# Kernel optimization log

Measured on AMD Instinct MI355X. Metric: run time of the kernel, lower is better.

The kernel has to match this reference:

```python
import jax, jax.numpy as jnp
import numpy as np

BETA = 0.1
IGNORE_INDEX = -100
B, T, H, V = 4, 512, 2048, 32000


def setup_inputs() -> dict:
    key = jax.random.key(0)
    k1, k2, k3, k4, k5 = jax.random.split(key, 5)
    x = jax.random.normal(k1, (B, T, H), dtype=jnp.float32)
    ref_x = jax.random.normal(k2, (B, T, H), dtype=jnp.float32)
    y = jax.random.randint(k3, (B, T), 0, V, dtype=jnp.int64)
    W = jax.random.normal(k4, (V, H), dtype=jnp.float32) * 0.02
    ref_W = jax.random.normal(k5, (V, H), dtype=jnp.float32) * 0.02
    return {"x": x, "ref_x": ref_x, "y": y, "W": W, "ref_W": ref_W}


def _avg_logps(inp, weight, target):
    # inp: [B,T,H], weight: [V,H], target: [B,T]
    logits = jnp.einsum('bth,vh->btv', inp, weight)          # [B,T,V]
    lse = jax.nn.logsumexp(logits, axis=-1)                  # [B,T]
    mask = (target != IGNORE_INDEX)
    safe = jnp.where(mask, target, 0)
    tok = jnp.take_along_axis(logits, safe[..., None], axis=-1)[..., 0]
    per_token_logps = tok - lse                               # [B,T]
    mask_f = mask.astype(per_token_logps.dtype)
    return (per_token_logps * mask_f).sum(-1) / mask_f.sum(-1)  # [B]


def reference(x, ref_x, y, W, ref_W):
    half = y.shape[0] // 2
    policy_logps = _avg_logps(x, W, y)
    # reference model runs under no_grad in the original
    ref_logps = jax.lax.stop_gradient(_avg_logps(ref_x, ref_W, y))
    logratios = policy_logps - ref_logps                      # [B]
    kl = jnp.zeros((), dtype=logratios.dtype)                 # kl=None -> 0
    chosen_losses = 1.0 - jax.nn.sigmoid(BETA * (logratios[:half] - kl))
    rejected_losses = 1.0 - jax.nn.sigmoid(BETA * (kl - logratios[half:]))
    return (chosen_losses.sum() + rejected_losses.sum()) / half
```

## Files before the change

kernel.cpp:

```cpp
#include <hip/hip_runtime.h>
#include <stdint.h>

#define B_DIM 4
#define T_DIM 512
#define NTOK  2048
#define H_DIM 2048
#define V_DIM 32000
#define TM    128
#define TN    128
#define BK    64
#define NCHUNK (V_DIM / TN)
#define NTILE  (NTOK / TM)
#define BETA   0.1f
#define IGNORE_INDEX (-100)

typedef _Float16 f16;
typedef _Float16 half8 __attribute__((ext_vector_type(8)));
typedef float    f32x4 __attribute__((ext_vector_type(4)));

__global__ __launch_bounds__(256) void cvt_f32_f16(const float* __restrict__ src,
                                                   f16* __restrict__ dst, int n) {
    int i = (blockIdx.x * 256 + threadIdx.x) * 8;
    if (i + 8 > n) return;
    float4 v0 = *(const float4*)(src + i);
    float4 v1 = *(const float4*)(src + i + 4);
    half8 h = { (f16)v0.x, (f16)v0.y, (f16)v0.z, (f16)v0.w,
                (f16)v1.x, (f16)v1.y, (f16)v1.z, (f16)v1.w };
    *(half8*)(dst + i) = h;
}

template <bool DIRECT>
__global__ __launch_bounds__(256, 3) void gemm_lse(
    const void* __restrict__ x0, const void* __restrict__ x1,
    const void* __restrict__ w0, const void* __restrict__ w1,
    const int* __restrict__ y,
    float2* __restrict__ pMS,
    float* __restrict__ tokL)
{
    const int tile  = blockIdx.x;
    const int chunk = blockIdx.y;
    const int model = blockIdx.z;
    const void* Xp = model ? x1 : x0;
    const void* Wp = model ? w1 : w0;

    const int tid  = threadIdx.x;
    const int lane = tid & 63;
    const int wave = tid >> 6;
    const int wm   = wave >> 1;
    const int wn   = wave & 1;

    __shared__ __align__(16) f16 As[8][TM][8];
    __shared__ __align__(16) f16 Bs[8][TN][8];
    __shared__ float redM[TM][2];
    __shared__ float redS[TM][2];
    __shared__ int   ys[TM];

    if (tid < TM) ys[tid] = y[tile * TM + tid];

    f32x4 acc[4][4];
#pragma unroll
    for (int i = 0; i < 4; ++i)
#pragma unroll
        for (int j = 0; j < 4; ++j) acc[i][j] = (f32x4){0.f, 0.f, 0.f, 0.f};

    const int rowA0 = tile * TM;
    const int rowB0 = chunk * TN;
    const int kc    = lane >> 4;

    const int rS = tid & 127;
    const int cS = tid >> 7;

    if (DIRECT) {
        const f16* pA = (const f16*)Xp + (size_t)(rowA0 + rS) * H_DIM + cS * 8;
        const f16* pB = (const f16*)Wp + (size_t)(rowB0 + rS) * H_DIM + cS * 8;
        f16* dA = &As[0][0][0] + tid * 8;
        f16* dB = &Bs[0][0][0] + tid * 8;

        for (int k0 = 0; k0 < H_DIM; k0 += BK) {
#pragma unroll
            for (int i = 0; i < 4; ++i)
                __builtin_amdgcn_global_load_lds(
                    (const __attribute__((address_space(1))) unsigned int*)(pA + i * 16),
                    (__attribute__((address_space(3))) unsigned int*)(dA + i * 2048),
                    16, 0, 0);
#pragma unroll
            for (int i = 0; i < 4; ++i)
                __builtin_amdgcn_global_load_lds(
                    (const __attribute__((address_space(1))) unsigned int*)(pB + i * 16),
                    (__attribute__((address_space(3))) unsigned int*)(dB + i * 2048),
                    16, 0, 0);
            pA += BK; pB += BK;
            __syncthreads();

#pragma unroll
            for (int p = 0; p < 2; ++p) {
                half8 af[4], bfr[4];
#pragma unroll
                for (int i = 0; i < 4; ++i)
                    af[i] = *(const half8*)As[p * 4 + kc][wm * 64 + i * 16 + (lane & 15)];
#pragma unroll
                for (int j = 0; j < 4; ++j)
                    bfr[j] = *(const half8*)Bs[p * 4 + kc][wn * 64 + j * 16 + (lane & 15)];
#pragma unroll
                for (int i = 0; i < 4; ++i)
#pragma unroll
                    for (int j = 0; j < 4; ++j)
                        acc[i][j] = __builtin_amdgcn_mfma_f32_16x16x32_f16(af[i], bfr[j], acc[i][j], 0, 0, 0);
            }
            __syncthreads();
        }
    } else {
        const float* pA = (const float*)Xp + (size_t)(rowA0 + rS) * H_DIM + cS * 8;
        const float* pB = (const float*)Wp + (size_t)(rowB0 + rS) * H_DIM + cS * 8;
        f16* dA = &As[0][0][0] + tid * 8;
        f16* dB = &Bs[0][0][0] + tid * 8;

        for (int k0 = 0; k0 < H_DIM; k0 += BK) {
#pragma unroll
            for (int i = 0; i < 4; ++i) {
                float4 v0 = *(const float4*)(pA + i * 16);
                float4 v1 = *(const float4*)(pA + i * 16 + 4);
                half8 h = { (f16)v0.x, (f16)v0.y, (f16)v0.z, (f16)v0.w,
                            (f16)v1.x, (f16)v1.y, (f16)v1.z, (f16)v1.w };
                *(half8*)(dA + i * 2048) = h;
            }
#pragma unroll
            for (int i = 0; i < 4; ++i) {
                float4 v0 = *(const float4*)(pB + i * 16);
                float4 v1 = *(const float4*)(pB + i * 16 + 4);
                half8 h = { (f16)v0.x, (f16)v0.y, (f16)v0.z, (f16)v0.w,
                            (f16)v1.x, (f16)v1.y, (f16)v1.z, (f16)v1.w };
                *(half8*)(dB + i * 2048) = h;
            }
            pA += BK; pB += BK;
            __syncthreads();

#pragma unroll
            for (int p = 0; p < 2; ++p) {
                half8 af[4], bfr[4];
#pragma unroll
                for (int i = 0; i < 4; ++i)
                    af[i] = *(const half8*)As[p * 4 + kc][wm * 64 + i * 16 + (lane & 15)];
#pragma unroll
                for (int j = 0; j < 4; ++j)
                    bfr[j] = *(const half8*)Bs[p * 4 + kc][wn * 64 + j * 16 + (lane & 15)];
#pragma unroll
                for (int i = 0; i < 4; ++i)
#pragma unroll
                    for (int j = 0; j < 4; ++j)
                        acc[i][j] = __builtin_amdgcn_mfma_f32_16x16x32_f16(af[i], bfr[j], acc[i][j], 0, 0, 0);
            }
            __syncthreads();
        }
    }

#pragma unroll
    for (int i = 0; i < 4; ++i) {
#pragma unroll
        for (int r = 0; r < 4; ++r) {
            int rl = wm * 64 + i * 16 + ((lane >> 4) << 2) + r;
            int t = ys[rl];
            int trel = t - (rowB0 + wn * 64);
#pragma unroll
            for (int j = 0; j < 4; ++j) {
                if (trel == j * 16 + (lane & 15))
                    tokL[model * NTOK + rowA0 + rl] = acc[i][j][r];
            }
        }
    }

#pragma unroll
    for (int i = 0; i < 4; ++i) {
#pragma unroll
        for (int r = 0; r < 4; ++r) {
            float mx = fmaxf(fmaxf(acc[i][0][r], acc[i][1][r]),
                             fmaxf(acc[i][2][r], acc[i][3][r]));
            for (int m = 1; m < 16; m <<= 1) mx = fmaxf(mx, __shfl_xor(mx, m, 64));
            float s = 0.f;
#pragma unroll
            for (int j = 0; j < 4; ++j) s += __expf(acc[i][j][r] - mx);
            for (int m = 1; m < 16; m <<= 1) s += __shfl_xor(s, m, 64);
            if ((lane & 15) == 0) {
                int rl = wm * 64 + i * 16 + ((lane >> 4) << 2) + r;
                redM[rl][wn] = mx;
                redS[rl][wn] = s;
            }
        }
    }
    __syncthreads();
    if (tid < TM) {
        float m0 = redM[tid][0], m1 = redM[tid][1];
        float s0 = redS[tid][0], s1 = redS[tid][1];
        float M = fmaxf(m0, m1);
        float S = s0 * __expf(m0 - M) + s1 * __expf(m1 - M);
        size_t o = ((size_t)model * NTOK + rowA0 + tid) * NCHUNK + chunk;
        pMS[o] = make_float2(M, S);
    }
}

__global__ __launch_bounds__(256) void lse_reduce(const float2* __restrict__ pMS,
                                                  const float* __restrict__ tokL,
                                                  const int* __restrict__ y,
                                                  float* __restrict__ logp) {
    int g = blockIdx.x * 4 + (threadIdx.x >> 6);
    int lane = threadIdx.x & 63;
    const float2* base = pMS + (size_t)g * NCHUNK;
    float M = -1e30f, S = 0.f;
    for (int c = lane; c < NCHUNK; c += 64) {
        float2 ms = base[c];
        if (ms.x > M) { S = S * __expf(M - ms.x) + ms.y; M = ms.x; }
        else          { S += ms.y * __expf(ms.x - M); }
    }
#pragma unroll
    for (int off = 1; off < 64; off <<= 1) {
        float Mo = __shfl_xor(M, off, 64);
        float So = __shfl_xor(S, off, 64);
        float Mn = fmaxf(M, Mo);
        S = S * __expf(M - Mn) + So * __expf(Mo - Mn);
        M = Mn;
    }
    if (lane == 0) {
        float lse = M + logf(S);
        int token = g & (NTOK - 1);
        int t = y[token];
        logp[g] = (t == IGNORE_INDEX) ? 0.f : (tokL[g] - lse);
    }
}

__device__ __forceinline__ float sigf(float z) { return 1.f / (1.f + expf(-z)); }

__global__ void final_loss(const float* __restrict__ logp,
                           const int* __restrict__ y,
                           float* __restrict__ out) {
    int lane = threadIdx.x;
    float avg[2][4];
    for (int model = 0; model < 2; ++model)
        for (int b = 0; b < 4; ++b) {
            float s = 0.f, c = 0.f;
            for (int t = lane; t < T_DIM; t += 64) {
                int token = b * T_DIM + t;
                if (y[token] != IGNORE_INDEX) { s += logp[model * NTOK + token]; c += 1.f; }
            }
            for (int m = 1; m < 64; m <<= 1) {
                s += __shfl_xor(s, m, 64);
                c += __shfl_xor(c, m, 64);
            }
            avg[model][b] = s / c;
        }
    if (lane == 0) {
        float loss = 0.f;
        for (int b = 0; b < 2; ++b) {
            float lr = avg[0][b] - avg[1][b];
            loss += 1.f - sigf(BETA * lr);
        }
        for (int b = 2; b < 4; ++b) {
            float lr = avg[0][b] - avg[1][b];
            loss += 1.f - sigf(-BETA * lr);
        }
        out[0] = loss * 0.5f;
    }
}

extern "C" void kernel_launch(void* const* d_in, const int* in_sizes, int n_in,
                              void* d_out, int out_size, void* d_ws, size_t ws_size,
                              hipStream_t stream) {
    const float* x  = (const float*)d_in[0];
    const float* rx = (const float*)d_in[1];
    const int*   y  = (const int*)d_in[2];
    const float* W  = (const float*)d_in[3];
    const float* rW = (const float*)d_in[4];
    float* out = (float*)d_out;

    const size_t nX = (size_t)NTOK * H_DIM;
    const size_t nW = (size_t)V_DIM * H_DIM;

    char* p = (char*)d_ws;
    float2* pMS = (float2*)p; p += (size_t)2 * NTOK * NCHUNK * 8;
    float* tokL = (float*)p;  p += (size_t)2 * NTOK * 4;
    float* logp = (float*)p;  p += (size_t)2 * NTOK * 4;
    size_t base = (size_t)(p - (char*)d_ws);
    size_t need_fast = base + 2 * nX * 2 + 2 * nW * 2;

    dim3 grid(NTILE, NCHUNK, 2);
    if (ws_size >= need_fast) {
        f16* xb  = (f16*)p; p += nX * 2;
        f16* rxb = (f16*)p; p += nX * 2;
        f16* wb  = (f16*)p; p += nW * 2;
        f16* rwb = (f16*)p; p += nW * 2;
        cvt_f32_f16<<<(int)(nX / 8 / 256), 256, 0, stream>>>(x,  xb,  (int)nX);
        cvt_f32_f16<<<(int)(nX / 8 / 256), 256, 0, stream>>>(rx, rxb, (int)nX);
        cvt_f32_f16<<<(int)(nW / 8 / 256), 256, 0, stream>>>(W,  wb,  (int)nW);
        cvt_f32_f16<<<(int)(nW / 8 / 256), 256, 0, stream>>>(rW, rwb, (int)nW);
        gemm_lse<true><<<grid, 256, 0, stream>>>(xb, rxb, wb, rwb, y, pMS, tokL);
    } else {
        gemm_lse<false><<<grid, 256, 0, stream>>>(x, rx, W, rW, y, pMS, tokL);
    }
    lse_reduce<<<1024, 256, 0, stream>>>(pMS, tokL, y, logp);
    final_loss<<<1, 64, 0, stream>>>(logp, y, out);
}
```

Measured before the change: 1.566 ms.

## Rewrite fp16 GEMM-LSE as 256x256 tile, 8-wave double-buffered pipelined kernel

Replaces the 128x128, 4-wave fp16 GEMM with a 256x256 tile kernel using 512 threads. It double-buffers LDS and issues async global-to-LDS loads interleaved with MFMA phases, using explicit barriers, waitcnts and setprio. The block index is remapped so that blocks sharing a weight chunk are grouped, and per-chunk max/sum partials halve in count. This targets memory stalls and load/compute serialization, at the cost of large LDS use (128KB), heavy register pressure from 32 accumulators, and fragile hand scheduling.

```diff
diff --git a/kernel.cpp b/kernel.cpp
--- a/kernel.cpp
+++ b/kernel.cpp
@@ -6,17 +6,22 @@
 #define NTOK  2048
 #define H_DIM 2048
 #define V_DIM 32000
+#define BETA   0.1f
+#define IGNORE_INDEX (-100)
+
 #define TM    128
 #define TN    128
 #define BK    64
-#define NCHUNK (V_DIM / TN)
-#define NTILE  (NTOK / TM)
-#define BETA   0.1f
-#define IGNORE_INDEX (-100)
+#define NCHUNK 250
+#define NCH8  125
+#define NTILE8 8
 
 typedef _Float16 f16;
 typedef _Float16 half8 __attribute__((ext_vector_type(8)));
 typedef float    f32x4 __attribute__((ext_vector_type(4)));
+
+#define AS1(p) ((const __attribute__((address_space(1))) unsigned int*)(p))
+#define AS3(p) ((__attribute__((address_space(3))) unsigned int*)(p))
 
 __global__ __launch_bounds__(256) void cvt_f32_f16(const float* __restrict__ src,
                                                    f16* __restrict__ dst, int n) {
@@ -29,10 +34,183 @@
     *(half8*)(dst + i) = h;
 }
 
-template <bool DIRECT>
-__global__ __launch_bounds__(256, 3) void gemm_lse(
-    const void* __restrict__ x0, const void* __restrict__ x1,
-    const void* __restrict__ w0, const void* __restrict__ w1,
+
+#define DSR_(d, a, OFFSTR) \
+    asm volatile("ds_read_b128 %0, %1 offset:" OFFSTR : "=v"(d) : "v"(a))
+
+#define VM4    asm volatile("s_waitcnt vmcnt(4)" ::: "memory")
+#define VMNONE ((void)0)
+
+#define STAGE(MAT, BUF, KH, KT, PTR) do {                                      \
+    const f16* s_ = (PTR) + (((KT) & 31) << 6) + (KH) * 32;                    \
+    f16* d_ = dBase + (BUF) * 32768 + (MAT) * 16384 + (KH) * 8192;             \
+    __builtin_amdgcn_global_load_lds(AS1(s_),      AS3(d_),        16, 0, 0);  \
+    __builtin_amdgcn_global_load_lds(AS1(s_ + 16), AS3(d_ + 4096), 16, 0, 0);  \
+} while (0)
+
+#define PHASE(BUF, KH, FH, WAITV, ...) do {                                    \
+    half8 af[4];                                                               \
+    unsigned aAd = A_rd + ((BUF) * 65536u + (KH) * 16384u + (FH) * 1024u);     \
+    DSR_(af[0], aAd, "0");   DSR_(af[1], aAd, "256");                          \
+    DSR_(af[2], aAd, "512"); DSR_(af[3], aAd, "768");                          \
+    if ((FH) == 0) {                                                           \
+        unsigned bAd = B_rd + ((BUF) * 65536u + (KH) * 16384u);                \
+        DSR_(bfp[0], bAd, "0");   DSR_(bfp[1], bAd, "256");                    \
+        DSR_(bfp[2], bAd, "512"); DSR_(bfp[3], bAd, "768");                    \
+    }                                                                          \
+    __VA_ARGS__;                                                               \
+    __builtin_amdgcn_sched_barrier(0);                                         \
+    __builtin_amdgcn_s_barrier();                                              \
+    __builtin_amdgcn_sched_barrier(0);                                         \
+    asm volatile("s_waitcnt lgkmcnt(0)" ::: "memory");                         \
+    __builtin_amdgcn_sched_barrier(0);                                         \
+    __builtin_amdgcn_s_setprio(1);                                             \
+    _Pragma("unroll")                                                          \
+    for (int m_ = 0; m_ < 4; ++m_) {                                           \
+        _Pragma("unroll")                                                      \
+        for (int n_ = 0; n_ < 4; ++n_)                                         \
+            acc[(FH) * 4 + m_][n_] = __builtin_amdgcn_mfma_f32_16x16x32_f16(   \
+                af[m_], bfp[n_], acc[(FH) * 4 + m_][n_], 0, 0, 0);             \
+    }                                                                          \
+    __builtin_amdgcn_s_setprio(0);                                             \
+    __builtin_amdgcn_sched_barrier(0);                                         \
+    WAITV;                                                                     \
+    __builtin_amdgcn_s_barrier();                                              \
+    __builtin_amdgcn_sched_barrier(0);                                         \
+} while (0)
+
+__global__ __launch_bounds__(512, 2) void gemm_lse8(
+    const f16* __restrict__ x0, const f16* __restrict__ x1,
+    const f16* __restrict__ w0, const f16* __restrict__ w1,
+    const int* __restrict__ y,
+    float2* __restrict__ pMS,
+    float* __restrict__ tokL)
+{
+    const int orig = blockIdx.x;
+    const int wg   = (orig & 7) * 250 + (orig >> 3);
+    const int tile = wg & 7;
+    const int rest = wg >> 3;
+    const int chunk = rest % NCH8;
+    const int model = rest / NCH8;
+
+    const f16* Xp = model ? x1 : x0;
+    const f16* Wp = model ? w1 : w0;
+
+    const int tid  = threadIdx.x;
+    const int lane = tid & 63;
+    const int wave = tid >> 6;
+    const int wm   = wave >> 2;
+    const int wn   = wave & 3;
+
+    __shared__ __align__(16) f16 sm[2][2][8][256][8];
+    __shared__ float redM[256][4];
+    __shared__ float redS[256][4];
+    __shared__ int   ys[256];
+
+    const int rowA0 = tile * 256;
+    const int rowB0 = chunk * 256;
+
+    f32x4 acc[8][4];
+#pragma unroll
+    for (int i = 0; i < 8; ++i)
+#pragma unroll
+        for (int j = 0; j < 4; ++j) acc[i][j] = (f32x4){0.f, 0.f, 0.f, 0.f};
+
+    const int rS = tid & 255;
+    const int cS = tid >> 8;
+    const f16* pA = Xp + (size_t)(rowA0 + rS) * H_DIM + cS * 8;
+    const f16* pB = Wp + (size_t)(rowB0 + rS) * H_DIM + cS * 8;
+    f16* dBase = &sm[0][0][0][0][0] + (size_t)tid * 8;
+
+    auto* smp3 = (__attribute__((address_space(3))) f16*)&sm[0][0][0][0][0];
+    const unsigned smBase = (unsigned)(uintptr_t)smp3;
+    const unsigned A_rd = smBase + ((unsigned)(lane >> 4) << 12)
+                        + (((unsigned)(wm * 128 + (lane & 15))) << 4);
+    const unsigned B_rd = smBase + 32768u + ((unsigned)(lane >> 4) << 12)
+                        + (((unsigned)(wn * 64 + (lane & 15))) << 4);
+
+    half8 bfp[4];
+
+    int yreg = 0;
+    if (tid < 256) yreg = y[rowA0 + tid];
+    asm volatile("s_waitcnt vmcnt(0)" ::: "memory");
+    __builtin_amdgcn_sched_barrier(0);
+
+    STAGE(0, 0, 0, 0, pA); STAGE(1, 0, 0, 0, pB);
+    STAGE(0, 0, 1, 0, pA); STAGE(1, 0, 1, 0, pB);
+    STAGE(0, 1, 0, 1, pA); STAGE(1, 1, 0, 1, pB);
+    asm volatile("s_waitcnt vmcnt(4)" ::: "memory");
+    __builtin_amdgcn_sched_barrier(0);
+    __builtin_amdgcn_s_barrier();
+    __builtin_amdgcn_sched_barrier(0);
+    if (tid < 256) ys[tid] = yreg;
+
+#pragma unroll 1
+    for (int i = 0; i < 16; ++i) {
+        const int kt1 = 2 * i + 1, kt2 = 2 * i + 2, kt3 = 2 * i + 3;
+        PHASE(0, 0, 0, VMNONE, STAGE(0, 1, 1, kt1, pA));
+        PHASE(0, 0, 1, VMNONE, STAGE(1, 1, 1, kt1, pB));
+        PHASE(0, 1, 0, VMNONE, STAGE(0, 0, 0, kt2, pA));
+        PHASE(0, 1, 1, VM4,    STAGE(1, 0, 0, kt2, pB));
+        PHASE(1, 0, 0, VMNONE, STAGE(0, 0, 1, kt2, pA));
+        PHASE(1, 0, 1, VMNONE, STAGE(1, 0, 1, kt2, pB));
+        PHASE(1, 1, 0, VMNONE, STAGE(0, 1, 0, kt3, pA));
+        PHASE(1, 1, 1, VM4,    STAGE(1, 1, 0, kt3, pB));
+    }
+
+    __syncthreads();
+
+#pragma unroll
+    for (int i2 = 0; i2 < 8; ++i2) {
+#pragma unroll
+        for (int r = 0; r < 4; ++r) {
+            int rl = wm * 128 + i2 * 16 + ((lane >> 4) << 2) + r;
+            int t = ys[rl];
+            int trel = t - (rowB0 + wn * 64);
+#pragma unroll
+            for (int j = 0; j < 4; ++j) {
+                if (trel == j * 16 + (lane & 15))
+                    tokL[model * NTOK + rowA0 + rl] = acc[i2][j][r];
+            }
+        }
+    }
+
+#pragma unroll
+    for (int i2 = 0; i2 < 8; ++i2) {
+#pragma unroll
+        for (int r = 0; r < 4; ++r) {
+            float mx = fmaxf(fmaxf(acc[i2][0][r], acc[i2][1][r]),
+                             fmaxf(acc[i2][2][r], acc[i2][3][r]));
+            for (int m = 1; m < 16; m <<= 1) mx = fmaxf(mx, __shfl_xor(mx, m, 64));
+            float s = 0.f;
+#pragma unroll
+            for (int j = 0; j < 4; ++j) s += __expf(acc[i2][j][r] - mx);
+            for (int m = 1; m < 16; m <<= 1) s += __shfl_xor(s, m, 64);
+            if ((lane & 15) == 0) {
+                int rl = wm * 128 + i2 * 16 + ((lane >> 4) << 2) + r;
+                redM[rl][wn] = mx;
+                redS[rl][wn] = s;
+            }
+        }
+    }
+    __syncthreads();
+    if (tid < 256) {
+        float M = redM[tid][0], S = redS[tid][0];
+#pragma unroll
+        for (int q = 1; q < 4; ++q) {
+            float m2 = redM[tid][q], s2 = redS[tid][q];
+            float Mn = fmaxf(M, m2);
+            S = S * __expf(M - Mn) + s2 * __expf(m2 - Mn);
+            M = Mn;
+        }
+        size_t o = ((size_t)model * NTOK + rowA0 + tid) * NCH8 + chunk;
+        pMS[o] = make_float2(M, S);
+    }
+}
+
+__global__ __launch_bounds__(256, 3) void gemm_lse_f32(
+    const float* __restrict__ x0, const float* __restrict__ x1,
+    const float* __restrict__ w0, const float* __restrict__ w1,
     const int* __restrict__ y,
     float2* __restrict__ pMS,
     float* __restrict__ tokL)
@@ -40,8 +218,8 @@
     const int tile  = blockIdx.x;
     const int chunk = blockIdx.y;
     const int model = blockIdx.z;
-    const void* Xp = model ? x1 : x0;
-    const void* Wp = model ? w1 : w0;
+    const float* Xp = model ? x1 : x0;
+    const float* Wp = model ? w1 : w0;
 
     const int tid  = threadIdx.x;
     const int lane = tid & 63;
@@ -66,92 +244,50 @@
     const int rowA0 = tile * TM;
     const int rowB0 = chunk * TN;
     const int kc    = lane >> 4;
-
     const int rS = tid & 127;
     const int cS = tid >> 7;
 
-    if (DIRECT) {
-        const f16* pA = (const f16*)Xp + (size_t)(rowA0 + rS) * H_DIM + cS * 8;
-        const f16* pB = (const f16*)Wp + (size_t)(rowB0 + rS) * H_DIM + cS * 8;
-        f16* dA = &As[0][0][0] + tid * 8;
-        f16* dB = &Bs[0][0][0] + tid * 8;
-
-        for (int k0 = 0; k0 < H_DIM; k0 += BK) {
+    const float* pA = Xp + (size_t)(rowA0 + rS) * H_DIM + cS * 8;
+    const float* pB = Wp + (size_t)(rowB0 + rS) * H_DIM + cS * 8;
+    f16* dA = &As[0][0][0] + tid * 8;
+    f16* dB = &Bs[0][0][0] + tid * 8;
+
+    for (int k0 = 0; k0 < H_DIM; k0 += BK) {
+#pragma unroll
+        for (int i = 0; i < 4; ++i) {
+            float4 v0 = *(const float4*)(pA + i * 16);
+            float4 v1 = *(const float4*)(pA + i * 16 + 4);
+            half8 h = { (f16)v0.x, (f16)v0.y, (f16)v0.z, (f16)v0.w,
+                        (f16)v1.x, (f16)v1.y, (f16)v1.z, (f16)v1.w };
+            *(half8*)(dA + i * 2048) = h;
+        }
+#pragma unroll
+        for (int i = 0; i < 4; ++i) {
+            float4 v0 = *(const float4*)(pB + i * 16);
+            float4 v1 = *(const float4*)(pB + i * 16 + 4);
+            half8 h = { (f16)v0.x, (f16)v0.y, (f16)v0.z, (f16)v0.w,
+                        (f16)v1.x, (f16)v1.y, (f16)v1.z, (f16)v1.w };
+            *(half8*)(dB + i * 2048) = h;
+        }
+        pA += BK; pB += BK;
+        __syncthreads();
+
+#pragma unroll
+        for (int p = 0; p < 2; ++p) {
+            half8 af[4], bfr[4];
 #pragma unroll
             for (int i = 0; i < 4; ++i)
-                __builtin_amdgcn_global_load_lds(
-                    (const __attribute__((address_space(1))) unsigned int*)(pA + i * 16),
-                    (__attribute__((address_space(3))) unsigned int*)(dA + i * 2048),
-                    16, 0, 0);
+                af[i] = *(const half8*)As[p * 4 + kc][wm * 64 + i * 16 + (lane & 15)];
+#pragma unroll
+            for (int j = 0; j < 4; ++j)
+                bfr[j] = *(const half8*)Bs[p * 4 + kc][wn * 64 + j * 16 + (lane & 15)];
 #pragma unroll
             for (int i = 0; i < 4; ++i)
-                __builtin_amdgcn_global_load_lds(
-                    (const __attribute__((address_space(1))) unsigned int*)(pB + i * 16),
-                    (__attribute__((address_space(3))) unsigned int*)(dB + i * 2048),
-                    16, 0, 0);
-            pA += BK; pB += BK;
-            __syncthreads();
-
-#pragma unroll
-            for (int p = 0; p < 2; ++p) {
-                half8 af[4], bfr[4];
-#pragma unroll
-                for (int i = 0; i < 4; ++i)
-                    af[i] = *(const half8*)As[p * 4 + kc][wm * 64 + i * 16 + (lane & 15)];
 #pragma unroll
                 for (int j = 0; j < 4; ++j)
-                    bfr[j] = *(const half8*)Bs[p * 4 + kc][wn * 64 + j * 16 + (lane & 15)];
-#pragma unroll
-                for (int i = 0; i < 4; ++i)
-#pragma unroll
-                    for (int j = 0; j < 4; ++j)
-                        acc[i][j] = __builtin_amdgcn_mfma_f32_16x16x32_f16(af[i], bfr[j], acc[i][j], 0, 0, 0);
-            }
-            __syncthreads();
-        }
-    } else {
-        const float* pA = (const float*)Xp + (size_t)(rowA0 + rS) * H_DIM + cS * 8;
-        const float* pB = (const float*)Wp + (size_t)(rowB0 + rS) * H_DIM + cS * 8;
-        f16* dA = &As[0][0][0] + tid * 8;
-        f16* dB = &Bs[0][0][0] + tid * 8;
-
-        for (int k0 = 0; k0 < H_DIM; k0 += BK) {
-#pragma unroll
-            for (int i = 0; i < 4; ++i) {
-                float4 v0 = *(const float4*)(pA + i * 16);
-                float4 v1 = *(const float4*)(pA + i * 16 + 4);
-                half8 h = { (f16)v0.x, (f16)v0.y, (f16)v0.z, (f16)v0.w,
-                            (f16)v1.x, (f16)v1.y, (f16)v1.z, (f16)v1.w };
-                *(half8*)(dA + i * 2048) = h;
-            }
-#pragma unroll
-            for (int i = 0; i < 4; ++i) {
-                float4 v0 = *(const float4*)(pB + i * 16);
-                float4 v1 = *(const float4*)(pB + i * 16 + 4);
-                half8 h = { (f16)v0.x, (f16)v0.y, (f16)v0.z, (f16)v0.w,
-                            (f16)v1.x, (f16)v1.y, (f16)v1.z, (f16)v1.w };
-                *(half8*)(dB + i * 2048) = h;
-            }
-            pA += BK; pB += BK;
-            __syncthreads();
-
-#pragma unroll
-            for (int p = 0; p < 2; ++p) {
-                half8 af[4], bfr[4];
-#pragma unroll
-                for (int i = 0; i < 4; ++i)
-                    af[i] = *(const half8*)As[p * 4 + kc][wm * 64 + i * 16 + (lane & 15)];
-#pragma unroll
-                for (int j = 0; j < 4; ++j)
-                    bfr[j] = *(const half8*)Bs[p * 4 + kc][wn * 64 + j * 16 + (lane & 15)];
-#pragma unroll
-                for (int i = 0; i < 4; ++i)
-#pragma unroll
-                    for (int j = 0; j < 4; ++j)
-                        acc[i][j] = __builtin_amdgcn_mfma_f32_16x16x32_f16(af[i], bfr[j], acc[i][j], 0, 0, 0);
-            }
-            __syncthreads();
-        }
+                    acc[i][j] = __builtin_amdgcn_mfma_f32_16x16x32_f16(af[i], bfr[j], acc[i][j], 0, 0, 0);
+        }
+        __syncthreads();
     }
 
 #pragma unroll
@@ -193,7 +329,7 @@
         float s0 = redS[tid][0], s1 = redS[tid][1];
         float M = fmaxf(m0, m1);
         float S = s0 * __expf(m0 - M) + s1 * __expf(m1 - M);
-        size_t o = ((size_t)model * NTOK + rowA0 + tid) * NCHUNK + chunk;
+        size_t o = ((size_t)model * NTOK + tile * TM + tid) * NCHUNK + chunk;
         pMS[o] = make_float2(M, S);
     }
 }
@@ -201,12 +337,13 @@
 __global__ __launch_bounds__(256) void lse_reduce(const float2* __restrict__ pMS,
                                                   const float* __restrict__ tokL,
                                                   const int* __restrict__ y,
-                                                  float* __restrict__ logp) {
+                                                  float* __restrict__ logp,
+                                                  int nchunk) {
     int g = blockIdx.x * 4 + (threadIdx.x >> 6);
     int lane = threadIdx.x & 63;
-    const float2* base = pMS + (size_t)g * NCHUNK;
+    const float2* base = pMS + (size_t)g * nchunk;
     float M = -1e30f, S = 0.f;
-    for (int c = lane; c < NCHUNK; c += 64) {
+    for (int c = lane; c < nchunk; c += 64) {
         float2 ms = base[c];
         if (ms.x > M) { S = S * __expf(M - ms.x) + ms.y; M = ms.x; }
         else          { S += ms.y * __expf(ms.x - M); }
@@ -281,7 +418,6 @@
     size_t base = (size_t)(p - (char*)d_ws);
     size_t need_fast = base + 2 * nX * 2 + 2 * nW * 2;
 
-    dim3 grid(NTILE, NCHUNK, 2);
     if (ws_size >= need_fast) {
         f16* xb  = (f16*)p; p += nX * 2;
         f16* rxb = (f16*)p; p += nX * 2;
@@ -291,10 +427,11 @@
         cvt_f32_f16<<<(int)(nX / 8 / 256), 256, 0, stream>>>(rx, rxb, (int)nX);
         cvt_f32_f16<<<(int)(nW / 8 / 256), 256, 0, stream>>>(W,  wb,  (int)nW);
         cvt_f32_f16<<<(int)(nW / 8 / 256), 256, 0, stream>>>(rW, rwb, (int)nW);
-        gemm_lse<true><<<grid, 256, 0, stream>>>(xb, rxb, wb, rwb, y, pMS, tokL);
+        gemm_lse8<<<dim3(NTILE8 * NCH8 * 2), 512, 0, stream>>>(xb, rxb, wb, rwb, y, pMS, tokL);
+        lse_reduce<<<1024, 256, 0, stream>>>(pMS, tokL, y, logp, NCH8);
     } else {
-        gemm_lse<false><<<grid, 256, 0, stream>>>(x, rx, W, rW, y, pMS, tokL);
-    }
-    lse_reduce<<<1024, 256, 0, stream>>>(pMS, tokL, y, logp);
+        gemm_lse_f32<<<dim3(NTOK / TM, NCHUNK, 2), 256, 0, stream>>>(x, rx, W, rW, y, pMS, tokL);
+        lse_reduce<<<1024, 256, 0, stream>>>(pMS, tokL, y, logp, NCHUNK);
+    }
     final_loss<<<1, 64, 0, stream>>>(logp, y, out);
 }
```

Measured after the change: 1.410 ms. 10.0% less time.
